# Kernel tuning notes

Measured on AMD Instinct MI355X. Metric: run time of the kernel, lower is better.

## Reference

```python
import jax, jax.numpy as jnp
import numpy as np

N_NODES = 50000
N_EDGES = 800000
D_IN = 64
D_OUT = 64


def setup_inputs() -> dict:
    key = jax.random.key(0)
    k_x, k_s, k_d, k_w, k_b = jax.random.split(key, 5)
    x = jax.random.normal(k_x, (N_NODES, D_IN), dtype=jnp.float32)
    src = jax.random.randint(k_s, (N_EDGES,), 0, N_NODES, dtype=jnp.int64)
    dst = jax.random.randint(k_d, (N_EDGES,), 0, N_NODES, dtype=jnp.int64)
    W = jax.random.normal(k_w, (D_OUT, D_IN), dtype=jnp.float32) / np.sqrt(D_IN)
    b = jax.random.normal(k_b, (D_OUT,), dtype=jnp.float32) * 0.01
    return {"x": x, "src": src, "dst": dst, "W": W, "b": b}


def reference(x, src, dst, W, b):
    # update_all(copy_u('h','m'), mean('m','h')): for each node v,
    # h[v] = mean over incoming edges (u->v) of x[u]; 0 if in-degree == 0.
    msgs = x[src]  # [E, D_IN] gather (irregular access)
    summed = jax.ops.segment_sum(msgs, dst, num_segments=N_NODES)  # [N, D_IN]
    deg = jax.ops.segment_sum(jnp.ones((src.shape[0],), dtype=x.dtype), dst,
                              num_segments=N_NODES)  # [N]
    h = summed / jnp.maximum(deg, 1.0)[:, None]  # zero-degree nodes stay 0
    # dense linear: h @ W.T + b
    return jnp.einsum("nd,od->no", h, W) + b
```

## Files before the change

### kernel.cpp

```cpp
#include <hip/hip_runtime.h>

#define N_NODES 50000
#define N_EDGES 800000
#define SLOTS 64
#define ZROW 50000
#define XROWS 50048
#define NBUCKET 196
#define BNODES 256
#define CAP 8192
#define NCHUNK 256
#define CE 3125
#define NCVT 400000
#define NTILES 3125

typedef short bf16x8 __attribute__((ext_vector_type(8)));
typedef float f32x4 __attribute__((ext_vector_type(4)));

__device__ __forceinline__ unsigned short f2bf(float f) {
    unsigned int u = __float_as_uint(f);
    unsigned int r = (u + 0x7fffu + ((u >> 16) & 1u)) >> 16;
    return (unsigned short)r;
}
__device__ __forceinline__ float bflo(unsigned int u) { return __uint_as_float(u << 16); }
__device__ __forceinline__ float bfhi(unsigned int u) { return __uint_as_float(u & 0xffff0000u); }

__global__ __launch_bounds__(256)
void gcn_bin(const int* __restrict__ src, const int* __restrict__ dst,
             const float4* __restrict__ x4,
             unsigned int* __restrict__ pbuf, int* __restrict__ gcur,
             uint4* __restrict__ xb) {
    __shared__ int hist[4][NBUCKET];
    __shared__ int wpre[4][NBUCKET];
    __shared__ int gbase[NBUCKET];
    int tid = threadIdx.x;
    int wid = tid >> 6;
    int chunk = blockIdx.x;
    for (int i = tid; i < 4 * NBUCKET; i += 256) ((int*)hist)[i] = 0;
    __syncthreads();

    int lo = chunk * CE;
    unsigned int pairr[13];
    unsigned int kp[13];
#pragma unroll
    for (int j = 0; j < 13; ++j) {
        int off = tid + j * 256;
        kp[j] = 0xFFFFFFFFu;
        if (off < CE) {
            int d = dst[lo + off];
            int s = src[lo + off];
            int key = d >> 8;
            int pos = atomicAdd(&hist[wid][key], 1);
            pairr[j] = ((unsigned int)d << 16) | (unsigned int)s;
            kp[j] = ((unsigned int)key << 16) | (unsigned int)pos;
        }
    }
    __syncthreads();
    if (tid < NBUCKET) {
        int c0 = hist[0][tid], c1 = hist[1][tid];
        int c2 = hist[2][tid], c3 = hist[3][tid];
        wpre[0][tid] = 0;
        wpre[1][tid] = c0;
        wpre[2][tid] = c0 + c1;
        wpre[3][tid] = c0 + c1 + c2;
        gbase[tid] = atomicAdd(&gcur[tid], c0 + c1 + c2 + c3);
    }
    __syncthreads();
#pragma unroll
    for (int j = 0; j < 13; ++j) {
        if (kp[j] != 0xFFFFFFFFu) {
            int key = (int)(kp[j] >> 16);
            int idx = gbase[key] + wpre[wid][key] + (int)(kp[j] & 0xFFFFu);
            if (idx < CAP) pbuf[key * CAP + idx] = pairr[j];
        }
    }

    int gi = chunk * 256 + tid;
    if (gi < 8) xb[(size_t)ZROW * 8 + gi] = make_uint4(0u, 0u, 0u, 0u);

    for (int i = gi; i < NCVT; i += NCHUNK * 256) {
        float4 a = x4[i * 2];
        float4 c = x4[i * 2 + 1];
        uint4 o;
        o.x = (unsigned)f2bf(a.x) | ((unsigned)f2bf(a.y) << 16);
        o.y = (unsigned)f2bf(a.z) | ((unsigned)f2bf(a.w) << 16);
        o.z = (unsigned)f2bf(c.x) | ((unsigned)f2bf(c.y) << 16);
        o.w = (unsigned)f2bf(c.z) | ((unsigned)f2bf(c.w) << 16);
        xb[i] = o;
    }
}

__global__ __launch_bounds__(256)
void gcn_build(const unsigned int* __restrict__ pbuf,
               const int* __restrict__ gcur,
               unsigned short* __restrict__ ell,
               unsigned short* __restrict__ deg) {
    __shared__ int cnt[BNODES];
    __shared__ unsigned short lell[BNODES * SLOTS];
    int key = blockIdx.x;
    int tid = threadIdx.x;
    cnt[tid] = 0;
    uint4* lf = (uint4*)lell;
    const uint4 pad = make_uint4(0xC350C350u, 0xC350C350u, 0xC350C350u, 0xC350C350u);
    for (int i = tid; i < BNODES * SLOTS / 8; i += 256) lf[i] = pad;
    __syncthreads();

    int m = min(gcur[key], CAP);
    int base = key * CAP;
    for (int i = tid; i < m; i += 256) {
        unsigned int u = pbuf[base + i];
        int dl = (int)(u >> 16) & 255;
        int pos = atomicAdd(&cnt[dl], 1);
        if (pos < SLOTS) lell[dl * SLOTS + pos] = (unsigned short)(u & 0xFFFFu);
    }
    __syncthreads();

    uint4* eg = (uint4*)(ell + (size_t)key * BNODES * SLOTS);
    const uint4* ls = (const uint4*)lell;
    for (int i = tid; i < BNODES * SLOTS / 8; i += 256) eg[i] = ls[i];
    deg[key * BNODES + tid] = (unsigned short)min(cnt[tid], SLOTS);
}

__global__ __launch_bounds__(256)
void gcn_gather_gemm(const uint4* __restrict__ xb4,
                     const unsigned short* __restrict__ deg,
                     const unsigned short* __restrict__ ell,
                     const float* __restrict__ W,
                     const float* __restrict__ b,
                     float* __restrict__ out) {
    __shared__ uint4 lh[16][9];
    int tid = threadIdx.x;
    int lane = tid & 63;
    int w = tid >> 6;
    int tile = blockIdx.x;
    int g = lane >> 3;
    int col = lane & 7;

#pragma unroll
    for (int i = 0; i < 4; ++i) {
        int node = tile * 16 + w * 4 + i;
        int c = (int)deg[node];
        int cr = (c + 7) & ~7;
        int myid = (int)ell[node * SLOTS + lane];

        float a0 = 0.f, a1 = 0.f, a2 = 0.f, a3 = 0.f;
        float a4 = 0.f, a5 = 0.f, a6 = 0.f, a7 = 0.f;
        for (int k = 0; k < cr; k += 8) {
            int sid = __shfl(myid, k + g, 64);
            uint4 v = xb4[sid * 8 + col];
            a0 += bflo(v.x); a1 += bfhi(v.x);
            a2 += bflo(v.y); a3 += bfhi(v.y);
            a4 += bflo(v.z); a5 += bfhi(v.z);
            a6 += bflo(v.w); a7 += bfhi(v.w);
        }
#pragma unroll
        for (int off = 8; off < 64; off <<= 1) {
            a0 += __shfl_xor(a0, off, 64); a1 += __shfl_xor(a1, off, 64);
            a2 += __shfl_xor(a2, off, 64); a3 += __shfl_xor(a3, off, 64);
            a4 += __shfl_xor(a4, off, 64); a5 += __shfl_xor(a5, off, 64);
            a6 += __shfl_xor(a6, off, 64); a7 += __shfl_xor(a7, off, 64);
        }
        if (g == 0) {
            float inv = c > 0 ? 1.0f / (float)c : 0.0f;
            uint4 o;
            o.x = (unsigned)f2bf(a0 * inv) | ((unsigned)f2bf(a1 * inv) << 16);
            o.y = (unsigned)f2bf(a2 * inv) | ((unsigned)f2bf(a3 * inv) << 16);
            o.z = (unsigned)f2bf(a4 * inv) | ((unsigned)f2bf(a5 * inv) << 16);
            o.w = (unsigned)f2bf(a6 * inv) | ((unsigned)f2bf(a7 * inv) << 16);
            lh[w * 4 + i][col] = o;
        }
    }
    __syncthreads();
    if (w != 0) return;

    int row = lane & 15;
    int quad = lane >> 4;
    int base = tile * 16;

    bf16x8 bfrag[4][2];
#pragma unroll
    for (int nt = 0; nt < 4; ++nt) {
#pragma unroll
        for (int kc = 0; kc < 2; ++kc) {
            const float* wp = &W[(nt * 16 + row) * 64 + kc * 32 + quad * 8];
            float4 w0 = *(const float4*)wp;
            float4 w1 = *(const float4*)(wp + 4);
            bf16x8 f;
            f[0] = (short)f2bf(w0.x); f[1] = (short)f2bf(w0.y);
            f[2] = (short)f2bf(w0.z); f[3] = (short)f2bf(w0.w);
            f[4] = (short)f2bf(w1.x); f[5] = (short)f2bf(w1.y);
            f[6] = (short)f2bf(w1.z); f[7] = (short)f2bf(w1.w);
            bfrag[nt][kc] = f;
        }
    }

    bf16x8 afrag[2];
#pragma unroll
    for (int kc = 0; kc < 2; ++kc) {
        uint4 av = lh[row][kc * 4 + quad];
        afrag[kc] = *(const bf16x8*)&av;
    }

    f32x4 d[4] = {{0.f, 0.f, 0.f, 0.f}, {0.f, 0.f, 0.f, 0.f},
                  {0.f, 0.f, 0.f, 0.f}, {0.f, 0.f, 0.f, 0.f}};
#pragma unroll
    for (int nt = 0; nt < 4; ++nt) {
#pragma unroll
        for (int kc = 0; kc < 2; ++kc) {
            d[nt] = __builtin_amdgcn_mfma_f32_16x16x32_bf16(
                afrag[kc], bfrag[nt][kc], d[nt], 0, 0, 0);
        }
    }

#pragma unroll
    for (int nt = 0; nt < 4; ++nt) {
        float bias = b[nt * 16 + row];
#pragma unroll
        for (int r = 0; r < 4; ++r) {
            out[(base + quad * 4 + r) * 64 + nt * 16 + row] = d[nt][r] + bias;
        }
    }
}

extern "C" void kernel_launch(void* const* d_in, const int* in_sizes, int n_in,
                              void* d_out, int out_size, void* d_ws, size_t ws_size,
                              hipStream_t stream) {
    const float* x   = (const float*)d_in[0];
    const int*   src = (const int*)d_in[1];
    const int*   dst = (const int*)d_in[2];
    const float* W   = (const float*)d_in[3];
    const float* b   = (const float*)d_in[4];
    float* out = (float*)d_out;

    unsigned int* pbuf = (unsigned int*)d_ws;
    int* gcur = (int*)(pbuf + (size_t)NBUCKET * CAP);
    unsigned short* ell = (unsigned short*)(gcur + 256);
    unsigned short* deg = ell + (size_t)NBUCKET * BNODES * SLOTS;
    unsigned short* xb  = deg + NBUCKET * BNODES;

    hipMemsetAsync(gcur, 0, 256 * sizeof(int), stream);
    gcn_bin<<<NCHUNK, 256, 0, stream>>>(src, dst, (const float4*)x,
                                        pbuf, gcur, (uint4*)xb);
    gcn_build<<<NBUCKET, 256, 0, stream>>>(pbuf, gcur, ell, deg);
    gcn_gather_gemm<<<NTILES, 256, 0, stream>>>(
        (const uint4*)xb, deg, ell, W, b, out);
}
```

Before: 66.58 us.

## Compact ELL adjacency into per-node offsets and split MFMA across all waves

Replaces the fixed 64-slot-per-node ELL table with a compacted neighbor list. Each node's slot count is rounded up to 8, prefix-scanned in the build kernel, and placed via a global atomic cursor, with a per-node offset array. This cuts build-kernel writes of padding and the gather kernel's index reads. The GEMM epilogue now spreads the four output column tiles across all four waves instead of running on one wave. The cost is a shared-memory scan with several barriers, an extra offset load per node, and order-dependent placement of node lists.

```diff
diff --git a/kernel.cpp b/kernel.cpp
--- a/kernel.cpp
+++ b/kernel.cpp
@@ -12,6 +12,7 @@
 #define CE 3125
 #define NCVT 400000
 #define NTILES 3125
+#define ELLC_CAP 1152000
 
 typedef short bf16x8 __attribute__((ext_vector_type(8)));
 typedef float f32x4 __attribute__((ext_vector_type(4)));
@@ -91,11 +92,14 @@
 
 __global__ __launch_bounds__(256)
 void gcn_build(const unsigned int* __restrict__ pbuf,
-               const int* __restrict__ gcur,
-               unsigned short* __restrict__ ell,
+               const int* __restrict__ gcur, int* __restrict__ ecur,
+               unsigned short* __restrict__ ellc,
+               unsigned int* __restrict__ offs,
                unsigned short* __restrict__ deg) {
     __shared__ int cnt[BNODES];
     __shared__ unsigned short lell[BNODES * SLOTS];
+    __shared__ int lpre[BNODES];
+    __shared__ int gbaseS;
     int key = blockIdx.x;
     int tid = threadIdx.x;
     cnt[tid] = 0;
@@ -114,16 +118,33 @@
     }
     __syncthreads();
 
-    uint4* eg = (uint4*)(ell + (size_t)key * BNODES * SLOTS);
-    const uint4* ls = (const uint4*)lell;
-    for (int i = tid; i < BNODES * SLOTS / 8; i += 256) eg[i] = ls[i];
-    deg[key * BNODES + tid] = (unsigned short)min(cnt[tid], SLOTS);
+    int c = min(cnt[tid], SLOTS);
+    int pl = (c + 7) & ~7;
+    lpre[tid] = pl;
+    __syncthreads();
+    for (int off = 1; off < 256; off <<= 1) {
+        int v = (tid >= off) ? lpre[tid - off] : 0;
+        __syncthreads();
+        lpre[tid] += v;
+        __syncthreads();
+    }
+    if (tid == 255) gbaseS = atomicAdd(ecur, lpre[255]);
+    __syncthreads();
+    int gb = gbaseS + lpre[tid] - pl;
+
+    offs[key * BNODES + tid] = (unsigned int)gb;
+    deg[key * BNODES + tid] = (unsigned short)c;
+
+    const uint4* lsrc = (const uint4*)&lell[tid * SLOTS];
+    uint4* gdst = (uint4*)&ellc[gb];
+    for (int j = 0; j < (pl >> 3); ++j) gdst[j] = lsrc[j];
 }
 
 __global__ __launch_bounds__(256)
 void gcn_gather_gemm(const uint4* __restrict__ xb4,
+                     const unsigned int* __restrict__ offs,
                      const unsigned short* __restrict__ deg,
-                     const unsigned short* __restrict__ ell,
+                     const unsigned short* __restrict__ ellc,
                      const float* __restrict__ W,
                      const float* __restrict__ b,
                      float* __restrict__ out) {
@@ -140,7 +161,8 @@
         int node = tile * 16 + w * 4 + i;
         int c = (int)deg[node];
         int cr = (c + 7) & ~7;
-        int myid = (int)ell[node * SLOTS + lane];
+        unsigned int off = offs[node];
+        int myid = (lane < cr) ? (int)ellc[off + lane] : ZROW;
 
         float a0 = 0.f, a1 = 0.f, a2 = 0.f, a3 = 0.f;
         float a4 = 0.f, a5 = 0.f, a6 = 0.f, a7 = 0.f;
@@ -153,11 +175,11 @@
             a6 += bflo(v.w); a7 += bfhi(v.w);
         }
 #pragma unroll
-        for (int off = 8; off < 64; off <<= 1) {
-            a0 += __shfl_xor(a0, off, 64); a1 += __shfl_xor(a1, off, 64);
-            a2 += __shfl_xor(a2, off, 64); a3 += __shfl_xor(a3, off, 64);
-            a4 += __shfl_xor(a4, off, 64); a5 += __shfl_xor(a5, off, 64);
-            a6 += __shfl_xor(a6, off, 64); a7 += __shfl_xor(a7, off, 64);
+        for (int off2 = 8; off2 < 64; off2 <<= 1) {
+            a0 += __shfl_xor(a0, off2, 64); a1 += __shfl_xor(a1, off2, 64);
+            a2 += __shfl_xor(a2, off2, 64); a3 += __shfl_xor(a3, off2, 64);
+            a4 += __shfl_xor(a4, off2, 64); a5 += __shfl_xor(a5, off2, 64);
+            a6 += __shfl_xor(a6, off2, 64); a7 += __shfl_xor(a7, off2, 64);
         }
         if (g == 0) {
             float inv = c > 0 ? 1.0f / (float)c : 0.0f;
@@ -170,27 +192,24 @@
         }
     }
     __syncthreads();
-    if (w != 0) return;
 
     int row = lane & 15;
     int quad = lane >> 4;
     int base = tile * 16;
-
-    bf16x8 bfrag[4][2];
-#pragma unroll
-    for (int nt = 0; nt < 4; ++nt) {
-#pragma unroll
-        for (int kc = 0; kc < 2; ++kc) {
-            const float* wp = &W[(nt * 16 + row) * 64 + kc * 32 + quad * 8];
-            float4 w0 = *(const float4*)wp;
-            float4 w1 = *(const float4*)(wp + 4);
-            bf16x8 f;
-            f[0] = (short)f2bf(w0.x); f[1] = (short)f2bf(w0.y);
-            f[2] = (short)f2bf(w0.z); f[3] = (short)f2bf(w0.w);
-            f[4] = (short)f2bf(w1.x); f[5] = (short)f2bf(w1.y);
-            f[6] = (short)f2bf(w1.z); f[7] = (short)f2bf(w1.w);
-            bfrag[nt][kc] = f;
-        }
+    int nt = w;
+
+    bf16x8 bfrag[2];
+#pragma unroll
+    for (int kc = 0; kc < 2; ++kc) {
+        const float* wp = &W[(nt * 16 + row) * 64 + kc * 32 + quad * 8];
+        float4 w0 = *(const float4*)wp;
+        float4 w1 = *(const float4*)(wp + 4);
+        bf16x8 f;
+        f[0] = (short)f2bf(w0.x); f[1] = (short)f2bf(w0.y);
+        f[2] = (short)f2bf(w0.z); f[3] = (short)f2bf(w0.w);
+        f[4] = (short)f2bf(w1.x); f[5] = (short)f2bf(w1.y);
+        f[6] = (short)f2bf(w1.z); f[7] = (short)f2bf(w1.w);
+        bfrag[kc] = f;
     }
 
     bf16x8 afrag[2];
@@ -200,24 +219,16 @@
         afrag[kc] = *(const bf16x8*)&av;
     }
 
-    f32x4 d[4] = {{0.f, 0.f, 0.f, 0.f}, {0.f, 0.f, 0.f, 0.f},
-                  {0.f, 0.f, 0.f, 0.f}, {0.f, 0.f, 0.f, 0.f}};
-#pragma unroll
-    for (int nt = 0; nt < 4; ++nt) {
-#pragma unroll
-        for (int kc = 0; kc < 2; ++kc) {
-            d[nt] = __builtin_amdgcn_mfma_f32_16x16x32_bf16(
-                afrag[kc], bfrag[nt][kc], d[nt], 0, 0, 0);
-        }
-    }
-
-#pragma unroll
-    for (int nt = 0; nt < 4; ++nt) {
-        float bias = b[nt * 16 + row];
-#pragma unroll
-        for (int r = 0; r < 4; ++r) {
-            out[(base + quad * 4 + r) * 64 + nt * 16 + row] = d[nt][r] + bias;
-        }
+    f32x4 d = {0.f, 0.f, 0.f, 0.f};
+#pragma unroll
+    for (int kc = 0; kc < 2; ++kc) {
+        d = __builtin_amdgcn_mfma_f32_16x16x32_bf16(afrag[kc], bfrag[kc], d, 0, 0, 0);
+    }
+
+    float bias = b[nt * 16 + row];
+#pragma unroll
+    for (int rr = 0; rr < 4; ++rr) {
+        out[(base + quad * 4 + rr) * 64 + nt * 16 + row] = d[rr] + bias;
     }
 }
 
@@ -233,14 +244,16 @@
 
     unsigned int* pbuf = (unsigned int*)d_ws;
     int* gcur = (int*)(pbuf + (size_t)NBUCKET * CAP);
-    unsigned short* ell = (unsigned short*)(gcur + 256);
-    unsigned short* deg = ell + (size_t)NBUCKET * BNODES * SLOTS;
-    unsigned short* xb  = deg + NBUCKET * BNODES;
-
-    hipMemsetAsync(gcur, 0, 256 * sizeof(int), stream);
+    int* ecur = gcur + 256;
+    unsigned int* offs = (unsigned int*)(gcur + 512);
+    unsigned short* deg = (unsigned short*)(offs + NBUCKET * BNODES);
+    unsigned short* ellc = deg + NBUCKET * BNODES;
+    unsigned short* xb = ellc + ELLC_CAP;
+
+    hipMemsetAsync(gcur, 0, 512 * sizeof(int), stream);
     gcn_bin<<<NCHUNK, 256, 0, stream>>>(src, dst, (const float4*)x,
                                         pbuf, gcur, (uint4*)xb);
-    gcn_build<<<NBUCKET, 256, 0, stream>>>(pbuf, gcur, ell, deg);
+    gcn_build<<<NBUCKET, 256, 0, stream>>>(pbuf, gcur, ecur, ellc, offs, deg);
     gcn_gather_gemm<<<NTILES, 256, 0, stream>>>(
-        (const uint4*)xb, deg, ell, W, b, out);
-}
+        (const uint4*)xb, offs, deg, ellc, W, b, out);
+}
```

Result: no change. 65.43 us (-1.7%).
